# Kernel tuning notes

Measured on AMD Instinct MI355X. Metric: run time of the kernel, lower is better.

## Reference

```python
import jax, jax.numpy as jnp
import numpy as np

N = 100000   # nodes
E = 1600000  # edges
D = 64       # input_size == hidden_size
L = 2        # n_layer


def setup_inputs() -> dict:
    key = jax.random.key(0)
    ks = jax.random.split(key, 16)
    s = 1.0 / np.sqrt(D)  # glorot-ish scale
    inp = jax.random.normal(ks[0], (N, D), jnp.float32)
    h = jax.random.normal(ks[1], (L, N, D), jnp.float32)
    edgidx = jax.random.randint(ks[2], (2, E), 0, N, jnp.int32)
    W = lambda i: jax.random.normal(ks[i], (L, D, D), jnp.float32) * s
    b = lambda i: jax.random.normal(ks[i], (L, D), jnp.float32) * 0.01
    return {
        'inp': inp, 'h': h, 'edgidx': edgidx,
        'Wxz': W(3), 'Whz': W(4), 'Wxr': W(5), 'Whr': W(6), 'Wxh': W(7), 'Whh': W(8),
        'bxz': b(9), 'bhz': b(10), 'bxr': b(11), 'bhr': b(12), 'bxh': b(13), 'bhh': b(14),
    }


def _gcn_norm(edgidx):
    # add self loops with weight 2 (improved=True), symmetric deg^-1/2 normalization
    row, col = edgidx[0], edgidx[1]
    loop = jnp.arange(N, dtype=row.dtype)
    row_f = jnp.concatenate([row, loop])
    col_f = jnp.concatenate([col, loop])
    w = jnp.concatenate([jnp.ones((E,), jnp.float32), 2.0 * jnp.ones((N,), jnp.float32)])
    deg = jax.ops.segment_sum(w, row_f, num_segments=N)
    dinv = jnp.where(deg > 0, deg ** -0.5, 0.0)
    norm = dinv[row_f] * w * dinv[col_f]
    return row_f, col_f, norm


def _gcn(x, Wt, bt, row_f, col_f, norm):
    # out[i] = sum_{(j->i)} norm_e * (x @ W)[j] + b   (PyG flow: gather at edge_index[0], scatter at edge_index[1])
    y = x @ Wt
    out = jax.ops.segment_sum(norm[:, None] * y[row_f], col_f, num_segments=N)
    return out + bt


def reference(inp, h, edgidx, Wxz, Whz, Wxr, Whr, Wxh, Whh, bxz, bhz, bxr, bhr, bxh, bhh):
    row_f, col_f, norm = _gcn_norm(edgidx)
    g = lambda x, W, b, i: _gcn(x, W[i], b[i], row_f, col_f, norm)
    x_in = inp
    outs = []
    for i in range(L):
        z = jax.nn.sigmoid(g(x_in, Wxz, bxz, i) + g(h[i], Whz, bhz, i))
        r = jax.nn.sigmoid(g(x_in, Wxr, bxr, i) + g(h[i], Whr, bhr, i))
        h_t = jnp.tanh(g(x_in, Wxh, bxh, i) + g(r * h[i], Whh, bhh, i))
        ho = z * h[i] + (1.0 - z) * h_t
        outs.append(ho)
        x_in = ho
    h_out = jnp.stack(outs)
    return (h_out, h_out)
```

## Files before the change

kernel.cpp:

```cpp
#include <hip/hip_runtime.h>
#include <hip/hip_fp16.h>
#include <math.h>
#include <stdint.h>

#define DD 64
#define NRG 512
#define BB  128

using f16x8 = __attribute__((ext_vector_type(8))) _Float16;
using f32x4 = __attribute__((ext_vector_type(4))) float;

static inline int divup(int a, int b){ return (a + b - 1) / b; }

__global__ __launch_bounds__(256) void bin_k(
    const int* __restrict__ edg, int E, int per, int nr, int cap,
    unsigned int* __restrict__ bufc, unsigned short* __restrict__ bufr,
    int* __restrict__ cntc, int* __restrict__ cntr)
{
  extern __shared__ int cur[];
  int* curc = cur;
  int* curr = cur + nr;
  const int b = blockIdx.x, t = threadIdx.x;
  for (int i = t; i < 2 * nr; i += 256) cur[i] = 0;
  __syncthreads();
  const int e0 = b * per;
  const int e1 = (e0 + per < E) ? e0 + per : E;
  unsigned int* mybufc = bufc + (size_t)b * nr * cap;
  unsigned short* mybufr = bufr + (size_t)b * nr * cap;
  for (int e = e0 + t; e < e1; e += 256){
    int r = edg[e];
    int c = edg[E + e];
    int rg = c >> 9;
    int p = atomicAdd(&curc[rg], 1);
    if (p < cap) mybufc[rg * cap + p] = ((unsigned int)r << 9) | (unsigned int)(c & 511);
    int rr = r >> 9;
    int q = atomicAdd(&curr[rr], 1);
    if (q < cap) mybufr[rr * cap + q] = (unsigned short)(r & 511);
  }
  __syncthreads();
  for (int i = t; i < nr; i += 256){
    int vc = curc[i]; cntc[b * nr + i] = vc < cap ? vc : cap;
    int vr = curr[i]; cntr[b * nr + i] = vr < cap ? vr : cap;
  }
}

__global__ __launch_bounds__(256) void cnt2b_k(
    const unsigned int* __restrict__ bufc, const unsigned short* __restrict__ bufr,
    const int* __restrict__ cntc, const int* __restrict__ cntr,
    int nb, int nr, int cap,
    int* __restrict__ locoff, int* __restrict__ rtot, float* __restrict__ dinv, int N)
{
  __shared__ int lhc[NRG];
  __shared__ int lhr[NRG];
  __shared__ int lcc[BB];
  __shared__ int lcr[BB];
  __shared__ int ps[256];
  const int rg = blockIdx.x, t = threadIdx.x;
  for (int i = t; i < NRG; i += 256){ lhc[i] = 0; lhr[i] = 0; }
  for (int i = t; i < nb; i += 256){ lcc[i] = cntc[i * nr + rg]; lcr[i] = cntr[i * nr + rg]; }
  __syncthreads();
  const int wv = t >> 6, lane = t & 63;
  for (int b = wv; b < nb; b += 4){
    const unsigned int* buf = bufc + ((size_t)b * nr + rg) * cap;
    int cnt = lcc[b];
    for (int i = lane; i < cnt; i += 64) atomicAdd(&lhc[buf[i] & 511], 1);
    const unsigned short* bufR = bufr + ((size_t)b * nr + rg) * cap;
    int cntR = lcr[b];
    for (int i = lane; i < cntR; i += 64) atomicAdd(&lhr[bufR[i]], 1);
  }
  __syncthreads();
  for (int i = t; i < NRG; i += 256){
    int node = rg * NRG + i;
    if (node < N) dinv[node] = rsqrtf((float)lhr[i] + 2.0f);
  }
  int v0 = lhc[2 * t], v1 = lhc[2 * t + 1];
  int s = v0 + v1;
  ps[t] = s; __syncthreads();
  for (int off = 1; off < 256; off <<= 1){
    int x = (t >= off) ? ps[t - off] : 0;
    __syncthreads();
    ps[t] += x;
    __syncthreads();
  }
  int excl = ps[t] - s;
  int n0 = rg * NRG + 2 * t;
  if (n0 < N)     locoff[n0]     = excl;
  if (n0 + 1 < N) locoff[n0 + 1] = excl + v0;
  if (t == 255) rtot[rg] = ps[255];
}

__global__ void rscan_k(const int* __restrict__ rtot, int* __restrict__ rbase,
                        int* __restrict__ offsets, int nr, int E, int N){
  __shared__ int sh[256];
  int t = threadIdx.x;
  int v = (t < nr) ? rtot[t] : 0;
  sh[t] = v; __syncthreads();
  for (int off = 1; off < 256; off <<= 1){
    int x = (t >= off) ? sh[t - off] : 0;
    __syncthreads();
    sh[t] += x;
    __syncthreads();
  }
  if (t < nr) rbase[t] = sh[t] - v;
  if (t == 0) offsets[N] = E;
}

__global__ __launch_bounds__(256) void scat_k(
    const unsigned int* __restrict__ bufc, const int* __restrict__ cntc,
    int nb, int nr, int cap, const int* __restrict__ locoff,
    const int* __restrict__ rbase,
    int* __restrict__ offsets, int* __restrict__ csr_src, int N)
{
  __shared__ int loff[NRG];
  __shared__ int lcc[BB];
  const int rg = blockIdx.x, t = threadIdx.x;
  const int base = rbase[rg];
  for (int i = t; i < NRG; i += 256){
    int node = rg * NRG + i;
    if (node < N){
      int o = base + locoff[node];
      loff[i] = o;
      offsets[node] = o;
    } else loff[i] = 0;
  }
  for (int i = t; i < nb; i += 256) lcc[i] = cntc[i * nr + rg];
  __syncthreads();
  const int wv = t >> 6, lane = t & 63;
  for (int b = wv; b < nb; b += 4){
    const unsigned int* buf = bufc + ((size_t)b * nr + rg) * cap;
    int cnt = lcc[b];
    for (int i = lane; i < cnt; i += 64){
      unsigned int v = buf[i];
      int p = atomicAdd(&loff[v & 511], 1);
      csr_src[p] = (int)(v >> 9);
    }
  }
}

__global__ void pack0_k(const float* __restrict__ X, const float* __restrict__ H,
                        const float* __restrict__ dinv, __half2* __restrict__ XH, int total){
  int i = blockIdx.x * 256 + threadIdx.x;
  if (i < total){
    float dv = dinv[i >> 6];
    __half2 v;
    v.x = __float2half_rn(dv * X[i]);
    v.y = __float2half_rn(dv * H[i]);
    XH[i] = v;
  }
}

__global__ void packb_k(const float* __restrict__ Wxz, const float* __restrict__ Whz,
                        const float* __restrict__ Wxr, const float* __restrict__ Whr,
                        const float* __restrict__ Wxh, const float* __restrict__ Whh,
                        const float* __restrict__ bxz, const float* __restrict__ bhz,
                        const float* __restrict__ bxr, const float* __restrict__ bhr,
                        const float* __restrict__ bxh, const float* __restrict__ bhh,
                        _Float16* __restrict__ Bg, _Float16* __restrict__ Bo,
                        float* __restrict__ biasg, int L){
  const int PER = 24576 + 4096 + 192;
  int tid = blockIdx.x * 256 + threadIdx.x;
  if (tid >= L * PER) return;
  int l = tid / PER, r = tid % PER;
  if (r < 24576){
    int q = r;
    int s = q & 7, lane = (q >> 3) & 63, ks = (q >> 9) & 3, jt = q >> 11;
    int k = ks * 32 + (lane >> 4) * 8 + s;
    int b = jt >> 2;
    int j = (jt & 3) * 16 + (lane & 15);
    const float* Wx = (b == 0) ? Wxz : (b == 1) ? Wxr : Wxh;
    const float* Wh = (b == 0) ? Whz : Whr;
    float v;
    if (k < 64) v = Wx[(size_t)l * 4096 + k * 64 + j];
    else        v = (b == 2) ? 0.0f : Wh[(size_t)l * 4096 + (k - 64) * 64 + j];
    Bg[(size_t)l * 24576 + q] = (_Float16)v;
  } else if (r < 24576 + 4096){
    int q = r - 24576;
    int s = q & 7, lane = (q >> 3) & 63, ks = (q >> 9) & 1, jt = q >> 10;
    int k = ks * 32 + (lane >> 4) * 8 + s;
    int j = jt * 16 + (lane & 15);
    Bo[(size_t)l * 4096 + q] = (_Float16)Whh[(size_t)l * 4096 + k * 64 + j];
  } else {
    int j = r - (24576 + 4096);
    int b = j >> 6, jj = j & 63;
    float v = (b == 0) ? bxz[l * 64 + jj] + bhz[l * 64 + jj]
            : (b == 1) ? bxr[l * 64 + jj] + bhr[l * 64 + jj]
                       : bxh[l * 64 + jj] + bhh[l * 64 + jj];
    biasg[l * 192 + j] = v;
  }
}

__global__ void agg2_k(const __half2* __restrict__ XH,
                       const int* __restrict__ offsets, const int* __restrict__ src,
                       const float* __restrict__ dinv,
                       _Float16* __restrict__ AXAH, int N){
  int wid = (blockIdx.x * blockDim.x + threadIdx.x) >> 6;
  int lane = threadIdx.x & 63;
  if (wid >= N) return;
  float dv = dinv[wid];
  size_t me = (size_t)wid * DD + lane;
  float2 sf = __half22float2(XH[me]);
  float ax[8], ah[8];
  #pragma unroll
  for (int j = 0; j < 8; j++){ ax[j] = 0.0f; ah[j] = 0.0f; }
  int s0 = offsets[wid], s1 = offsets[wid + 1];
  int e = s0;
  for (; e + 8 <= s1; e += 8){
    int sn[8];
    float2 f[8];
    #pragma unroll
    for (int j = 0; j < 8; j++) sn[j] = src[e + j];
    #pragma unroll
    for (int j = 0; j < 8; j++) f[j] = __half22float2(XH[(size_t)sn[j] * DD + lane]);
    #pragma unroll
    for (int j = 0; j < 8; j++){
      ax[j] += f[j].x;
      ah[j] += f[j].y;
    }
  }
  for (; e < s1; ++e){
    float2 fa = __half22float2(XH[(size_t)src[e] * DD + lane]);
    ax[0] += fa.x;
    ah[0] += fa.y;
  }
  float axs = ((ax[0] + ax[1]) + (ax[2] + ax[3])) + ((ax[4] + ax[5]) + (ax[6] + ax[7]));
  float ahs = ((ah[0] + ah[1]) + (ah[2] + ah[3])) + ((ah[4] + ah[5]) + (ah[6] + ah[7]));
  size_t o = (size_t)wid * 128 + lane;
  AXAH[o]      = (_Float16)(dv * (axs + 2.0f * sf.x));
  AXAH[o + 64] = (_Float16)(dv * (ahs + 2.0f * sf.y));
}

__global__ void agg1_k(const _Float16* __restrict__ RH,
                       const int* __restrict__ offsets, const int* __restrict__ src,
                       const float* __restrict__ dinv,
                       _Float16* __restrict__ Arh, int N){
  int wid = (blockIdx.x * blockDim.x + threadIdx.x) >> 6;
  int lane = threadIdx.x & 63;
  if (wid >= N) return;
  float dv = dinv[wid];
  size_t me = (size_t)wid * DD + lane;
  float selfv = (float)RH[me];
  float ax[8];
  #pragma unroll
  for (int j = 0; j < 8; j++) ax[j] = 0.0f;
  int s0 = offsets[wid], s1 = offsets[wid + 1];
  int e = s0;
  for (; e + 8 <= s1; e += 8){
    int sn[8];
    float f[8];
    #pragma unroll
    for (int j = 0; j < 8; j++) sn[j] = src[e + j];
    #pragma unroll
    for (int j = 0; j < 8; j++) f[j] = (float)RH[(size_t)sn[j] * DD + lane];
    #pragma unroll
    for (int j = 0; j < 8; j++) ax[j] += f[j];
  }
  for (; e < s1; ++e){
    ax[0] += (float)RH[(size_t)src[e] * DD + lane];
  }
  float axs = ((ax[0] + ax[1]) + (ax[2] + ax[3])) + ((ax[4] + ax[5]) + (ax[6] + ax[7]));
  Arh[me] = (_Float16)(dv * (axs + 2.0f * selfv));
}

__global__ __launch_bounds__(256) void gatem_k(
    const _Float16* __restrict__ AXAH, const float* __restrict__ Hh,
    const float* __restrict__ dinv,
    const _Float16* __restrict__ Bg, const float* __restrict__ biasg,
    _Float16* __restrict__ zb, _Float16* __restrict__ rhb,
    _Float16* __restrict__ t1b, int N)
{
  const int lane = threadIdx.x & 63;
  const int wv   = threadIdx.x >> 6;
  const long nbase = ((long)blockIdx.x * 4 + wv) * 32;
  if (nbase >= N) return;
  const int m  = lane & 15;
  const int kb = lane >> 4;

  f32x4 acc[2][12];
  #pragma unroll
  for (int jt = 0; jt < 12; jt++){
    float bv = biasg[jt * 16 + m];
    f32x4 b4 = {bv, bv, bv, bv};
    acc[0][jt] = b4;
    acc[1][jt] = b4;
  }

  #pragma unroll 1
  for (int ks = 0; ks < 4; ks++){
    f16x8 af0, af1;
    {
      long r0 = nbase + m;           if (r0 >= N) r0 = N - 1;
      long r1 = nbase + 16 + m;      if (r1 >= N) r1 = N - 1;
      af0 = *(const f16x8*)(AXAH + (size_t)r0 * 128 + ks * 32 + kb * 8);
      af1 = *(const f16x8*)(AXAH + (size_t)r1 * 128 + ks * 32 + kb * 8);
    }
    #pragma unroll
    for (int jt = 0; jt < 12; jt++){
      f16x8 bf = *(const f16x8*)(Bg + ((size_t)(jt * 4 + ks) * 64 + lane) * 8);
      acc[0][jt] = __builtin_amdgcn_mfma_f32_16x16x32_f16(af0, bf, acc[0][jt], 0, 0, 0);
      acc[1][jt] = __builtin_amdgcn_mfma_f32_16x16x32_f16(af1, bf, acc[1][jt], 0, 0, 0);
    }
  }

  #pragma unroll
  for (int mt = 0; mt < 2; mt++){
    #pragma unroll
    for (int i = 0; i < 4; i++){
      long row = nbase + mt * 16 + kb * 4 + i;
      if (row < N){
        float dvr = dinv[row];
        #pragma unroll
        for (int jq = 0; jq < 4; jq++){
          int j = jq * 16 + m;
          size_t o = (size_t)row * 64 + j;
          float zpre = acc[mt][jq][i];
          float rpre = acc[mt][4 + jq][i];
          float t1v  = acc[mt][8 + jq][i];
          float hv = Hh[o];
          zb[o]  = (_Float16)(1.0f / (1.0f + __expf(-zpre)));
          rhb[o] = (_Float16)(dvr * hv / (1.0f + __expf(-rpre)));
          t1b[o] = (_Float16)t1v;
        }
      }
    }
  }
}

__global__ __launch_bounds__(256) void outm_k(
    const _Float16* __restrict__ Arh, const _Float16* __restrict__ t1b,
    const _Float16* __restrict__ zb, const float* __restrict__ Hh,
    const float* __restrict__ dinv,
    const _Float16* __restrict__ Bo,
    float* __restrict__ o1, float* __restrict__ o2,
    const float* __restrict__ hNext, __half2* __restrict__ XHnext,
    int doPack, int N)
{
  const int lane = threadIdx.x & 63;
  const int wv   = threadIdx.x >> 6;
  const long nbase = ((long)blockIdx.x * 4 + wv) * 32;
  if (nbase >= N) return;
  const int m  = lane & 15;
  const int kb = lane >> 4;

  f32x4 acc[2][4];
  #pragma unroll
  for (int mt = 0; mt < 2; mt++){
    #pragma unroll
    for (int jt = 0; jt < 4; jt++){
      #pragma unroll
      for (int i = 0; i < 4; i++){
        long row = nbase + mt * 16 + kb * 4 + i;
        if (row >= N) row = N - 1;
        acc[mt][jt][i] = (float)t1b[(size_t)row * 64 + jt * 16 + m];
      }
    }
  }

  #pragma unroll
  for (int ks = 0; ks < 2; ks++){
    f16x8 af0, af1;
    {
      long r0 = nbase + m;           if (r0 >= N) r0 = N - 1;
      long r1 = nbase + 16 + m;      if (r1 >= N) r1 = N - 1;
      af0 = *(const f16x8*)(Arh + (size_t)r0 * 64 + ks * 32 + kb * 8);
      af1 = *(const f16x8*)(Arh + (size_t)r1 * 64 + ks * 32 + kb * 8);
    }
    #pragma unroll
    for (int jt = 0; jt < 4; jt++){
      f16x8 bf = *(const f16x8*)(Bo + ((size_t)(jt * 2 + ks) * 64 + lane) * 8);
      acc[0][jt] = __builtin_amdgcn_mfma_f32_16x16x32_f16(af0, bf, acc[0][jt], 0, 0, 0);
      acc[1][jt] = __builtin_amdgcn_mfma_f32_16x16x32_f16(af1, bf, acc[1][jt], 0, 0, 0);
    }
  }

  #pragma unroll
  for (int mt = 0; mt < 2; mt++){
    #pragma unroll
    for (int i = 0; i < 4; i++){
      long row = nbase + mt * 16 + kb * 4 + i;
      if (row < N){
        float dvr = dinv[row];
        #pragma unroll
        for (int jt = 0; jt < 4; jt++){
          int j = jt * 16 + m;
          size_t o = (size_t)row * 64 + j;
          float e = __expf(2.0f * acc[mt][jt][i]);
          float ht = 1.0f - 2.0f / (e + 1.0f);
          float z = (float)zb[o];
          float hv = Hh[o];
          float ho = z * hv + (1.0f - z) * ht;
          o1[o] = ho;
          o2[o] = ho;
          if (doPack){
            __half2 v;
            v.x = __float2half_rn(dvr * ho);
            v.y = __float2half_rn(dvr * hNext[o]);
            XHnext[o] = v;
          }
        }
      }
    }
  }
}

extern "C" void kernel_launch(void* const* d_in, const int* in_sizes, int n_in,
                              void* d_out, int out_size, void* d_ws, size_t ws_size,
                              hipStream_t stream){
  const float* inp = (const float*)d_in[0];
  const float* h   = (const float*)d_in[1];
  const int*   edg = (const int*)d_in[2];
  const float* Wxz = (const float*)d_in[3];
  const float* Whz = (const float*)d_in[4];
  const float* Wxr = (const float*)d_in[5];
  const float* Whr = (const float*)d_in[6];
  const float* Wxh = (const float*)d_in[7];
  const float* Whh = (const float*)d_in[8];
  const float* bxz = (const float*)d_in[9];
  const float* bhz = (const float*)d_in[10];
  const float* bxr = (const float*)d_in[11];
  const float* bhr = (const float*)d_in[12];
  const float* bxh = (const float*)d_in[13];
  const float* bhh = (const float*)d_in[14];
  float* out = (float*)d_out;

  const int ND = in_sizes[0];
  const int N  = ND / DD;
  const int E  = in_sizes[2] / 2;
  const int L  = in_sizes[1] / ND;

  const int nr  = divup(N, NRG);
  const int per = divup(E, BB);
  const int cap = (per / nr) * 3 + 64;

  char* p = (char*)d_ws;
  auto alloc = [&](size_t bytes) -> void* {
    void* r = (void*)p;
    p += ((bytes + 255) / 256) * 256;
    return r;
  };
  auto a256 = [](size_t b) -> size_t { return ((b + 255) / 256) * 256; };

  int*      offsets = (int*)alloc((size_t)(N + 1) * 4);
  int*      locoff  = (int*)alloc((size_t)N * 4);
  int*      rtot    = (int*)alloc(256 * 4);
  int*      rbase   = (int*)alloc(256 * 4);
  float*    dinv    = (float*)alloc((size_t)N * 4);
  int*      cntc    = (int*)alloc((size_t)BB * nr * 4);
  int*      cntr    = (int*)alloc((size_t)BB * nr * 4);
  int*      csr_src = (int*)alloc((size_t)E * 4);
  __half2*  XH      = (__half2*)alloc((size_t)ND * 4);
  _Float16* Bg      = (_Float16*)alloc((size_t)L * 24576 * 2);
  _Float16* Bo      = (_Float16*)alloc((size_t)L * 4096 * 2);
  float*    biasg   = (float*)alloc((size_t)L * 192 * 4);

  size_t bufc_b  = a256((size_t)BB * nr * cap * 4);
  size_t bufr_b  = a256((size_t)BB * nr * cap * 2);
  size_t axah_b  = a256((size_t)N * 128 * 2);
  size_t nd2_b   = a256((size_t)ND * 2);
  size_t ov_b    = axah_b + 4 * nd2_b;
  if (bufc_b + bufr_b > ov_b) ov_b = bufc_b + bufr_b;
  char* ov = (char*)alloc(ov_b);
  unsigned int*   bufc = (unsigned int*)ov;
  unsigned short* bufr = (unsigned short*)(ov + bufc_b);
  _Float16* AXAH = (_Float16*)ov;
  _Float16* Arh  = (_Float16*)(ov + axah_b);
  _Float16* zb   = (_Float16*)(ov + axah_b + nd2_b);
  _Float16* t1b  = (_Float16*)(ov + axah_b + 2 * nd2_b);
  _Float16* rhb  = (_Float16*)(ov + axah_b + 3 * nd2_b);

  bin_k<<<BB, 256, 2 * nr * 4, stream>>>(edg, E, per, nr, cap, bufc, bufr, cntc, cntr);
  cnt2b_k<<<nr, 256, 0, stream>>>(bufc, bufr, cntc, cntr, BB, nr, cap,
                                  locoff, rtot, dinv, N);
  rscan_k<<<1, 256, 0, stream>>>(rtot, rbase, offsets, nr, E, N);
  scat_k<<<nr, 256, 0, stream>>>(bufc, cntc, BB, nr, cap, locoff, rbase,
                                 offsets, csr_src, N);

  pack0_k<<<divup(ND, 256), 256, 0, stream>>>(inp, h, dinv, XH, ND);
  {
    const int PER = 24576 + 4096 + 192;
    packb_k<<<divup(L * PER, 256), 256, 0, stream>>>(
        Wxz, Whz, Wxr, Whr, Wxh, Whh,
        bxz, bhz, bxr, bhr, bxh, bhh, Bg, Bo, biasg, L);
  }

  const int aggBlocks = divup(N, 4);
  const int mBlocks   = divup(N, 128);

  for (int l = 0; l < L; l++){
    const float* Hh = h + (size_t)l * ND;
    agg2_k<<<aggBlocks, 256, 0, stream>>>(XH, offsets, csr_src, dinv, AXAH, N);
    gatem_k<<<mBlocks, 256, 0, stream>>>(AXAH, Hh, dinv,
        Bg + (size_t)l * 24576, biasg + (size_t)l * 192, zb, rhb, t1b, N);
    agg1_k<<<aggBlocks, 256, 0, stream>>>(rhb, offsets, csr_src, dinv, Arh, N);
    const int doPack = (l + 1 < L);
    outm_k<<<mBlocks, 256, 0, stream>>>(Arh, t1b, zb, Hh, dinv,
        Bo + (size_t)l * 4096,
        out + (size_t)l * ND, out + (size_t)L * ND + (size_t)l * ND,
        h + (size_t)(l + 1 < L ? l + 1 : l) * ND, XH, doPack, N);
  }
}
```

Before: 528.5 us.

## Store gate intermediates in MFMA fragment order and coalesce output writes via LDS

gatem_k now writes z, t1 and a precomputed z*h in per-thread MFMA fragment layout as contiguous 16-byte vectors. outm_k reads them back the same way, which removes the scattered fp16 reads and the fp32 h reload. The final outputs are staged through LDS so that o1, o2 and the packed next-layer XH can be written as float4 rows. The cost is extra workspace for fragment buffers, a padded LDS tile per wave, and one added intermediate array (z*h rounded to fp16, which slightly changes precision).

```diff
diff --git a/kernel.cpp b/kernel.cpp
--- a/kernel.cpp
+++ b/kernel.cpp
@@ -265,8 +265,8 @@
     const _Float16* __restrict__ AXAH, const float* __restrict__ Hh,
     const float* __restrict__ dinv,
     const _Float16* __restrict__ Bg, const float* __restrict__ biasg,
-    _Float16* __restrict__ zb, _Float16* __restrict__ rhb,
-    _Float16* __restrict__ t1b, int N)
+    _Float16* __restrict__ zbf, _Float16* __restrict__ zhf_g,
+    _Float16* __restrict__ rhb, _Float16* __restrict__ t1f, int N)
 {
   const int lane = threadIdx.x & 63;
   const int wv   = threadIdx.x >> 6;
@@ -301,59 +301,69 @@
     }
   }
 
+  _Float16 zf[32], tf[32], zhf[32];
   #pragma unroll
   for (int mt = 0; mt < 2; mt++){
     #pragma unroll
     for (int i = 0; i < 4; i++){
       long row = nbase + mt * 16 + kb * 4 + i;
-      if (row < N){
-        float dvr = dinv[row];
-        #pragma unroll
-        for (int jq = 0; jq < 4; jq++){
-          int j = jq * 16 + m;
-          size_t o = (size_t)row * 64 + j;
-          float zpre = acc[mt][jq][i];
-          float rpre = acc[mt][4 + jq][i];
-          float t1v  = acc[mt][8 + jq][i];
-          float hv = Hh[o];
-          zb[o]  = (_Float16)(1.0f / (1.0f + __expf(-zpre)));
-          rhb[o] = (_Float16)(dvr * hv / (1.0f + __expf(-rpre)));
-          t1b[o] = (_Float16)t1v;
-        }
+      long rc = row < N ? row : N - 1;
+      float dvr = dinv[rc];
+      #pragma unroll
+      for (int jq = 0; jq < 4; jq++){
+        int j = jq * 16 + m;
+        size_t o = (size_t)rc * 64 + j;
+        float hv = Hh[o];
+        float z  = 1.0f / (1.0f + __expf(-acc[mt][jq][i]));
+        float rr = 1.0f / (1.0f + __expf(-acc[mt][4 + jq][i]));
+        const int idx = mt * 16 + jq * 4 + i;
+        zf[idx]  = (_Float16)z;
+        zhf[idx] = (_Float16)(z * hv);
+        tf[idx]  = (_Float16)acc[mt][8 + jq][i];
+        if (row < N) rhb[o] = (_Float16)(dvr * hv * rr);
       }
     }
   }
+  const size_t fo = ((size_t)blockIdx.x * 256 + threadIdx.x) * 32;
+  #pragma unroll
+  for (int q = 0; q < 4; q++){
+    *(f16x8*)(zbf   + fo + 8 * q) = *(f16x8*)&zf[8 * q];
+    *(f16x8*)(t1f   + fo + 8 * q) = *(f16x8*)&tf[8 * q];
+    *(f16x8*)(zhf_g + fo + 8 * q) = *(f16x8*)&zhf[8 * q];
+  }
 }
 
 __global__ __launch_bounds__(256) void outm_k(
-    const _Float16* __restrict__ Arh, const _Float16* __restrict__ t1b,
-    const _Float16* __restrict__ zb, const float* __restrict__ Hh,
+    const _Float16* __restrict__ Arh, const _Float16* __restrict__ t1f,
+    const _Float16* __restrict__ zbf, const _Float16* __restrict__ zhf_g,
     const float* __restrict__ dinv,
     const _Float16* __restrict__ Bo,
     float* __restrict__ o1, float* __restrict__ o2,
     const float* __restrict__ hNext, __half2* __restrict__ XHnext,
     int doPack, int N)
 {
+  __shared__ float lds_os[4][16 * 65];
   const int lane = threadIdx.x & 63;
   const int wv   = threadIdx.x >> 6;
   const long nbase = ((long)blockIdx.x * 4 + wv) * 32;
   if (nbase >= N) return;
   const int m  = lane & 15;
   const int kb = lane >> 4;
+  const size_t fo = ((size_t)blockIdx.x * 256 + threadIdx.x) * 32;
+
+  _Float16 tf[32];
+  #pragma unroll
+  for (int q = 0; q < 4; q++)
+    *(f16x8*)&tf[8 * q] = *(const f16x8*)(t1f + fo + 8 * q);
 
   f32x4 acc[2][4];
   #pragma unroll
-  for (int mt = 0; mt < 2; mt++){
-    #pragma unroll
-    for (int jt = 0; jt < 4; jt++){
+  for (int mt = 0; mt < 2; mt++)
+    #pragma unroll
+    for (int jt = 0; jt < 4; jt++)
       #pragma unroll
-      for (int i = 0; i < 4; i++){
-        long row = nbase + mt * 16 + kb * 4 + i;
-        if (row >= N) row = N - 1;
-        acc[mt][jt][i] = (float)t1b[(size_t)row * 64 + jt * 16 + m];
-      }
-    }
-  }
+      for (int i = 0; i < 4; i++)
+        acc[mt][jt][i] = (float)tf[mt * 16 + jt * 4 + i];
 
   #pragma unroll
   for (int ks = 0; ks < 2; ks++){
@@ -372,31 +382,53 @@
     }
   }
 
+  _Float16 zf[32], zhf[32];
+  #pragma unroll
+  for (int q = 0; q < 4; q++){
+    *(f16x8*)&zf[8 * q]  = *(const f16x8*)(zbf   + fo + 8 * q);
+    *(f16x8*)&zhf[8 * q] = *(const f16x8*)(zhf_g + fo + 8 * q);
+  }
+
+  const int rl2 = lane >> 2;
+  const int c0  = (lane & 3) * 16;
+
   #pragma unroll
   for (int mt = 0; mt < 2; mt++){
     #pragma unroll
     for (int i = 0; i < 4; i++){
-      long row = nbase + mt * 16 + kb * 4 + i;
-      if (row < N){
-        float dvr = dinv[row];
-        #pragma unroll
-        for (int jt = 0; jt < 4; jt++){
-          int j = jt * 16 + m;
-          size_t o = (size_t)row * 64 + j;
-          float e = __expf(2.0f * acc[mt][jt][i]);
-          float ht = 1.0f - 2.0f / (e + 1.0f);
-          float z = (float)zb[o];
-          float hv = Hh[o];
-          float ho = z * hv + (1.0f - z) * ht;
-          o1[o] = ho;
-          o2[o] = ho;
-          if (doPack){
-            __half2 v;
-            v.x = __float2half_rn(dvr * ho);
-            v.y = __float2half_rn(dvr * hNext[o]);
-            XHnext[o] = v;
-          }
-        }
+      const int rl = kb * 4 + i;
+      #pragma unroll
+      for (int jt = 0; jt < 4; jt++){
+        const int idx = mt * 16 + jt * 4 + i;
+        float e  = __expf(2.0f * acc[mt][jt][i]);
+        float ht = 1.0f - 2.0f / (e + 1.0f);
+        float z  = (float)zf[idx];
+        lds_os[wv][rl * 65 + jt * 16 + m] = (float)zhf[idx] + (1.0f - z) * ht;
+      }
+    }
+    long grow = nbase + mt * 16 + rl2;
+    bool vr = grow < N;
+    long gc = vr ? grow : N - 1;
+    #pragma unroll
+    for (int q = 0; q < 4; q++){
+      float4 v = *(float4*)&lds_os[wv][rl2 * 65 + c0 + q * 4];
+      if (vr){
+        *(float4*)(o1 + gc * 64 + c0 + q * 4) = v;
+        *(float4*)(o2 + gc * 64 + c0 + q * 4) = v;
+      }
+    }
+    if (doPack && vr){
+      float dvr = dinv[gc];
+      #pragma unroll
+      for (int q = 0; q < 4; q++){
+        float4 hov = *(float4*)&lds_os[wv][rl2 * 65 + c0 + q * 4];
+        float4 hnv = *(const float4*)(hNext + gc * 64 + c0 + q * 4);
+        __half2 tmp[4];
+        tmp[0].x = __float2half_rn(dvr * hov.x); tmp[0].y = __float2half_rn(dvr * hnv.x);
+        tmp[1].x = __float2half_rn(dvr * hov.y); tmp[1].y = __float2half_rn(dvr * hnv.y);
+        tmp[2].x = __float2half_rn(dvr * hov.z); tmp[2].y = __float2half_rn(dvr * hnv.z);
+        tmp[3].x = __float2half_rn(dvr * hov.w); tmp[3].y = __float2half_rn(dvr * hnv.w);
+        *(float4*)(XHnext + gc * 64 + c0 + q * 4) = *(float4*)tmp;
       }
     }
   }
@@ -430,6 +462,7 @@
   const int nr  = divup(N, NRG);
   const int per = divup(E, BB);
   const int cap = (per / nr) * 3 + 64;
+  const int mBlocks = divup(N, 128);
 
   char* p = (char*)d_ws;
   auto alloc = [&](size_t bytes) -> void* {
@@ -456,16 +489,18 @@
   size_t bufr_b  = a256((size_t)BB * nr * cap * 2);
   size_t axah_b  = a256((size_t)N * 128 * 2);
   size_t nd2_b   = a256((size_t)ND * 2);
-  size_t ov_b    = axah_b + 4 * nd2_b;
+  size_t frag_b  = a256((size_t)mBlocks * 128 * 64 * 2);
+  size_t ov_b    = axah_b + 2 * nd2_b + 3 * frag_b;
   if (bufc_b + bufr_b > ov_b) ov_b = bufc_b + bufr_b;
   char* ov = (char*)alloc(ov_b);
   unsigned int*   bufc = (unsigned int*)ov;
   unsigned short* bufr = (unsigned short*)(ov + bufc_b);
   _Float16* AXAH = (_Float16*)ov;
   _Float16* Arh  = (_Float16*)(ov + axah_b);
-  _Float16* zb   = (_Float16*)(ov + axah_b + nd2_b);
-  _Float16* t1b  = (_Float16*)(ov + axah_b + 2 * nd2_b);
-  _Float16* rhb  = (_Float16*)(ov + axah_b + 3 * nd2_b);
+  _Float16* rhb  = (_Float16*)(ov + axah_b + nd2_b);
+  _Float16* zbf  = (_Float16*)(ov + axah_b + 2 * nd2_b);
+  _Float16* t1f  = (_Float16*)(ov + axah_b + 2 * nd2_b + frag_b);
+  _Float16* zhf  = (_Float16*)(ov + axah_b + 2 * nd2_b + 2 * frag_b);
 
   bin_k<<<BB, 256, 2 * nr * 4, stream>>>(edg, E, per, nr, cap, bufc, bufr, cntc, cntr);
   cnt2b_k<<<nr, 256, 0, stream>>>(bufc, bufr, cntc, cntr, BB, nr, cap,
@@ -483,16 +518,15 @@
   }
 
   const int aggBlocks = divup(N, 4);
-  const int mBlocks   = divup(N, 128);
 
   for (int l = 0; l < L; l++){
     const float* Hh = h + (size_t)l * ND;
     agg2_k<<<aggBlocks, 256, 0, stream>>>(XH, offsets, csr_src, dinv, AXAH, N);
     gatem_k<<<mBlocks, 256, 0, stream>>>(AXAH, Hh, dinv,
-        Bg + (size_t)l * 24576, biasg + (size_t)l * 192, zb, rhb, t1b, N);
+        Bg + (size_t)l * 24576, biasg + (size_t)l * 192, zbf, zhf, rhb, t1f, N);
     agg1_k<<<aggBlocks, 256, 0, stream>>>(rhb, offsets, csr_src, dinv, Arh, N);
     const int doPack = (l + 1 < L);
-    outm_k<<<mBlocks, 256, 0, stream>>>(Arh, t1b, zb, Hh, dinv,
+    outm_k<<<mBlocks, 256, 0, stream>>>(Arh, t1f, zbf, zhf, dinv,
         Bo + (size_t)l * 4096,
         out + (size_t)l * ND, out + (size_t)L * ND + (size_t)l * ND,
         h + (size_t)(l + 1 < L ? l + 1 : l) * ND, XH, doPack, N);
```

New measurement: 554.5 us. 1.05x slower.
